# Performance work log

Measured on AMD Instinct MI355X. Metric: run time of the kernel, lower is better.

## Reference

```python
import jax, jax.numpy as jnp
import numpy as np

NEG_INF = -1e9  # fp32-safe mask value for non-edges
ALPHA = 0.2     # LeakyReLU negative slope


def setup_inputs() -> dict:
    key = jax.random.key(0)
    k1, k2, k3, k4, k5 = jax.random.split(key, 5)
    N, F_in, H, F_out = 4096, 512, 8, 64
    features = jax.random.normal(k1, (N, F_in), dtype=jnp.float32)
    adjacency_matrix = jax.random.randint(k2, (N, N), 0, 2, dtype=jnp.int32)
    W = jax.random.normal(k3, (H, F_in, F_out), dtype=jnp.float32) * (F_in ** -0.5)
    a_src = jax.random.normal(k4, (H, F_out), dtype=jnp.float32) * (F_out ** -0.5)
    a_dst = jax.random.normal(k5, (H, F_out), dtype=jnp.float32) * (F_out ** -0.5)
    return {"features": features, "adjacency_matrix": adjacency_matrix,
            "W": W, "a_src": a_src, "a_dst": a_dst}


def reference(features, adjacency_matrix, W, a_src, a_dst):
    # Per-head linear projection: [H, N, F_out]
    Wh = jnp.einsum('nf,hfo->hno', features, W)
    # Attention logits e_ij = LeakyReLU(a_src . Wh_i + a_dst . Wh_j)
    src = jnp.einsum('hno,ho->hn', Wh, a_src)  # [H, N]
    dst = jnp.einsum('hno,ho->hn', Wh, a_dst)  # [H, N]
    e = jax.nn.leaky_relu(src[:, :, None] + dst[:, None, :], ALPHA)  # [H, N, N]
    mask = (adjacency_matrix > 0)[None, :, :]
    e = jnp.where(mask, e, jnp.asarray(NEG_INF, e.dtype))
    attn = jax.nn.softmax(e, axis=-1)  # adjacency-masked row softmax
    h = jnp.einsum('hij,hjo->hio', attn, Wh)  # [H, N, F_out]
    h = jax.nn.elu(h)
    # concat=True: torch.cat over feature dim -> [N, H*F_out]
    return jnp.transpose(h, (1, 0, 2)).reshape(h.shape[1], -1)
```

## Files before the change

kernel.cpp:

```cpp
#include <hip/hip_runtime.h>
#include <hip/hip_bf16.h>

typedef __bf16 bf16x8 __attribute__((ext_vector_type(8)));
typedef float  f32x4  __attribute__((ext_vector_type(4)));
typedef unsigned short u16x8 __attribute__((ext_vector_type(8)));
typedef unsigned short us4   __attribute__((ext_vector_type(4)));

#define HH    8
#define NN    4096
#define FIN   512
#define FOUT  64
#define ALPHA 0.2f

__global__ __launch_bounds__(256) void k_transpose_w(
    const float* __restrict__ Wsrc, __hip_bfloat16* __restrict__ WT) {
    __shared__ __hip_bfloat16 lt[64][65];
    const int h  = blockIdx.x >> 3;
    const int f0 = (blockIdx.x & 7) * 64;
    const int tid = threadIdx.x;
#pragma unroll
    for (int p = 0; p < 16; ++p) {
        int f = p * 4 + (tid >> 6);
        int o = tid & 63;
        lt[f][o] = __float2bfloat16(Wsrc[((size_t)h * FIN + f0 + f) * FOUT + o]);
    }
    __syncthreads();
#pragma unroll
    for (int p = 0; p < 16; ++p) {
        int o = p * 4 + (tid >> 6);
        int f = tid & 63;
        WT[((size_t)h * FOUT + o) * FIN + f0 + f] = lt[f][o];
    }
}

__global__ __launch_bounds__(256) void k_prep(
    int* __restrict__ adj,
    const float* __restrict__ feat,
    const __hip_bfloat16* __restrict__ WT,
    const float* __restrict__ a_src,
    const float* __restrict__ a_dst,
    unsigned short* __restrict__ WhT,
    float* __restrict__ srcv,
    unsigned short* __restrict__ Ebf, unsigned short* __restrict__ Fbf) {
    __shared__ alignas(16) __hip_bfloat16 lfeat[32][520];

    const int tid = threadIdx.x;

    if (blockIdx.x < 2048) {
        const size_t base = (size_t)blockIdx.x * 8192;
        unsigned m = 0;
#pragma unroll
        for (int p = 0; p < 8; ++p) {
            int4 v = *(const int4*)(adj + base + tid * 32 + p * 4);
            m |= (unsigned)(v.x > 0) << (p * 4);
            m |= (unsigned)(v.y > 0) << (p * 4 + 1);
            m |= (unsigned)(v.z > 0) << (p * 4 + 2);
            m |= (unsigned)(v.w > 0) << (p * 4 + 3);
        }
        __syncthreads();
        ((unsigned*)adj)[base + tid] = m;
        return;
    }

    const int pb   = blockIdx.x - 2048;
    const int tile = pb & 127;
    const int hgy  = pb >> 7;

#pragma unroll
    for (int p = 0; p < 16; ++p) {
        int idx  = p * 256 + tid;
        int row  = idx >> 7;
        int col4 = (idx & 127) * 4;
        float4 f = *(const float4*)(feat + (size_t)(tile * 32 + row) * FIN + col4);
        __hip_bfloat16* dst = &lfeat[row][col4];
        dst[0] = __float2bfloat16(f.x); dst[1] = __float2bfloat16(f.y);
        dst[2] = __float2bfloat16(f.z); dst[3] = __float2bfloat16(f.w);
    }
    __syncthreads();

    const int h     = hgy * 4 + (tid >> 6);
    const int lane  = tid & 63;
    const int row16 = lane & 15;
    const int quad  = lane >> 4;

    const unsigned short* WTu = (const unsigned short*)WT + (size_t)h * FOUT * FIN;

    f32x4 acc[2][4] = {};
    for (int k0 = 0; k0 < FIN; k0 += 32) {
        bf16x8 a0 = *(const bf16x8*)&lfeat[row16][k0 + quad * 8];
        bf16x8 a1 = *(const bf16x8*)&lfeat[16 + row16][k0 + quad * 8];
#pragma unroll
        for (int ot = 0; ot < 4; ++ot) {
            bf16x8 b = *(const bf16x8*)(WTu + (size_t)(ot * 16 + row16) * FIN + k0 + quad * 8);
            acc[0][ot] = __builtin_amdgcn_mfma_f32_16x16x32_bf16(a0, b, acc[0][ot], 0, 0, 0);
            acc[1][ot] = __builtin_amdgcn_mfma_f32_16x16x32_bf16(a1, b, acc[1][ot], 0, 0, 0);
        }
    }

#pragma unroll
    for (int g = 0; g < 2; ++g)
#pragma unroll
        for (int ot = 0; ot < 4; ++ot) {
            us4 u;
#pragma unroll
            for (int r = 0; r < 4; ++r)
                u[r] = __builtin_bit_cast(unsigned short, (__bf16)acc[g][ot][r]);
            *(us4*)(WhT + (size_t)(h * FOUT + ot * 16 + row16) * NN
                        + tile * 32 + g * 16 + quad * 4) = u;
        }

    float asv[4], adv[4];
#pragma unroll
    for (int ot = 0; ot < 4; ++ot) {
        asv[ot] = a_src[h * FOUT + ot * 16 + row16];
        adv[ot] = a_dst[h * FOUT + ot * 16 + row16];
    }
#pragma unroll
    for (int g = 0; g < 2; ++g)
#pragma unroll
        for (int r = 0; r < 4; ++r) {
            float ss = 0.f, dd = 0.f;
#pragma unroll
            for (int ot = 0; ot < 4; ++ot) {
                ss += acc[g][ot][r] * asv[ot];
                dd += acc[g][ot][r] * adv[ot];
            }
            ss += __shfl_xor(ss, 1); ss += __shfl_xor(ss, 2);
            ss += __shfl_xor(ss, 4); ss += __shfl_xor(ss, 8);
            dd += __shfl_xor(dd, 1); dd += __shfl_xor(dd, 2);
            dd += __shfl_xor(dd, 4); dd += __shfl_xor(dd, 8);
            if (row16 == 0) {
                int n = tile * 32 + g * 16 + quad * 4 + r;
                srcv[h * NN + n] = ss;
                __bf16 e = (__bf16)__expf(dd);
                __bf16 f = (__bf16)__expf(ALPHA * dd);
                Ebf[h * NN + n] = __builtin_bit_cast(unsigned short, e);
                Fbf[h * NN + n] = __builtin_bit_cast(unsigned short, f);
            }
        }
}

__global__ __launch_bounds__(512, 2) void k_flash(
    const unsigned* __restrict__ maskp,
    const float* __restrict__ srcv,
    const unsigned short* __restrict__ Ebf,
    const unsigned short* __restrict__ Fbf,
    const unsigned short* __restrict__ WhT,
    float* __restrict__ out) {
    __shared__ float st[2][128 * 68];
    __shared__ float lds_l[2][128];

    unsigned* lmask = (unsigned*)&st[0][0];

    const int tid   = threadIdx.x;
    const int seg   = tid >> 6;
    const int lane  = tid & 63;
    const int row16 = lane & 15;
    const int quad  = lane >> 4;
    const int shl   = quad * 8;
    const int tile  = blockIdx.x;
    const int h     = blockIdx.y;

#pragma unroll
    for (int p = 0; p < 8; ++p) {
        int tt = tid + p * 512;
        int c  = tt >> 6;
        int o  = (tt & 63) * 16;
        int4 v = *(const int4*)((const char*)maskp
                                + (size_t)(tile * 64 + c) * 32768 + o);
        int row = c * 2 + (o >> 9);
        int dw  = (o & 511) >> 2;
        *(int4*)&lmask[row * 132 + dw] = v;
    }
    __syncthreads();

    float Es[8], Fs[8];
#pragma unroll
    for (int g = 0; g < 8; ++g) {
        float si = srcv[h * NN + tile * 128 + g * 16 + row16];
        Es[g] = __expf(si);
        Fs[g] = __expf(ALPHA * si);
    }
    const int mbase = row16 * 132 + seg * 16;

    const unsigned short* Eb = Ebf + h * NN + seg * 512;
    const unsigned short* Fb = Fbf + h * NN + seg * 512;
    const unsigned short* wh = WhT + (size_t)h * FOUT * NN + seg * 512;

    f32x4 acc[8][4] = {};
    float lsum[8]   = {};

#pragma unroll 1
    for (int t = 0; t < 16; ++t) {
        int jj = t * 32 + shl;
        u16x8 ev = *(const u16x8*)(Eb + jj);
        u16x8 fv = *(const u16x8*)(Fb + jj);
        bf16x8 b[4];
#pragma unroll
        for (int ot = 0; ot < 4; ++ot)
            b[ot] = *(const bf16x8*)(wh + (size_t)(ot * 16 + row16) * NN + jj);

        float ef[8], ff[8];
#pragma unroll
        for (int k = 0; k < 8; ++k) {
            ef[k] = __uint_as_float((unsigned)ev[k] << 16);
            ff[k] = __uint_as_float((unsigned)fv[k] << 16);
        }

#pragma unroll
        for (int gp = 0; gp < 4; ++gp) {
            const int g0 = gp * 2, g1 = g0 + 1;
            unsigned mb0 = (lmask[mbase + g0 * 2112 + t] >> shl) & 0xffu;
            unsigned mb1 = (lmask[mbase + g1 * 2112 + t] >> shl) & 0xffu;
            union { bf16x8 v8; __hip_bfloat162 h2[4]; } a0u, a1u;
#pragma unroll
            for (int kk = 0; kk < 4; ++kk) {
                const int ka = kk * 2, kb = ka + 1;
                float p0a = ((mb0 >> ka) & 1u) ? fmaxf(ef[ka] * Es[g0], ff[ka] * Fs[g0]) : 0.f;
                float p0b = ((mb0 >> kb) & 1u) ? fmaxf(ef[kb] * Es[g0], ff[kb] * Fs[g0]) : 0.f;
                float p1a = ((mb1 >> ka) & 1u) ? fmaxf(ef[ka] * Es[g1], ff[ka] * Fs[g1]) : 0.f;
                float p1b = ((mb1 >> kb) & 1u) ? fmaxf(ef[kb] * Es[g1], ff[kb] * Fs[g1]) : 0.f;
                lsum[g0] += p0a + p0b;
                lsum[g1] += p1a + p1b;
                a0u.h2[kk] = __float22bfloat162_rn(make_float2(p0a, p0b));
                a1u.h2[kk] = __float22bfloat162_rn(make_float2(p1a, p1b));
            }
#pragma unroll
            for (int ot = 0; ot < 4; ++ot) {
                acc[g0][ot] = __builtin_amdgcn_mfma_f32_16x16x32_bf16(a0u.v8, b[ot], acc[g0][ot], 0, 0, 0);
                acc[g1][ot] = __builtin_amdgcn_mfma_f32_16x16x32_bf16(a1u.v8, b[ot], acc[g1][ot], 0, 0, 0);
            }
        }
    }

#pragma unroll
    for (int g = 0; g < 8; ++g) {
        lsum[g] += __shfl_xor(lsum[g], 16);
        lsum[g] += __shfl_xor(lsum[g], 32);
    }

    __syncthreads();

    auto stash = [&](int buf) {
#pragma unroll
        for (int g = 0; g < 8; ++g)
#pragma unroll
            for (int ot = 0; ot < 4; ++ot)
#pragma unroll
                for (int r = 0; r < 4; ++r)
                    st[buf][(g * 16 + quad * 4 + r) * 68 + ot * 16 + row16] = acc[g][ot][r];
        if (quad == 0)
#pragma unroll
            for (int g = 0; g < 8; ++g)
                lds_l[buf][g * 16 + row16] = lsum[g];
    };
    auto addin = [&](int buf) {
#pragma unroll
        for (int g = 0; g < 8; ++g) {
#pragma unroll
            for (int ot = 0; ot < 4; ++ot)
#pragma unroll
                for (int r = 0; r < 4; ++r)
                    acc[g][ot][r] += st[buf][(g * 16 + quad * 4 + r) * 68 + ot * 16 + row16];
            lsum[g] += lds_l[buf][g * 16 + row16];
        }
    };

    if (seg == 1) stash(0);
    if (seg == 3) stash(1);
    __syncthreads();
    if (seg == 0) addin(0);
    if (seg == 2) addin(1);
    __syncthreads();
    if (seg == 5) stash(0);
    if (seg == 7) stash(1);
    __syncthreads();
    if (seg == 4) addin(0);
    if (seg == 6) addin(1);
    __syncthreads();
    if (seg == 2) stash(0);
    if (seg == 6) stash(1);
    __syncthreads();
    if (seg == 0) addin(0);
    if (seg == 4) addin(1);
    __syncthreads();
    if (seg == 4) stash(0);
    __syncthreads();
    if (seg == 0) {
        addin(0);
#pragma unroll
        for (int g = 0; g < 8; ++g)
#pragma unroll
            for (int r = 0; r < 4; ++r) {
                int   qr  = quad * 4 + r;
                float l   = __shfl(lsum[g], qr);
                float rl  = 1.0f / l;
#pragma unroll
                for (int ot = 0; ot < 4; ++ot) {
                    float v = acc[g][ot][r] * rl;
                    float y = v > 0.f ? v : __expf(v) - 1.f;
                    st[0][(g * 16 + qr) * 68 + ot * 16 + row16] = y;
                }
            }
    }
    __syncthreads();
#pragma unroll
    for (int p = 0; p < 4; ++p) {
        int f    = tid + p * 512;
        int row  = f >> 4;
        int col4 = (f & 15) * 4;
        float4 v = *(const float4*)&st[0][row * 68 + col4];
        *(float4*)&out[(size_t)(tile * 128 + row) * (HH * FOUT) + h * FOUT + col4] = v;
    }
}

extern "C" void kernel_launch(void* const* d_in, const int* in_sizes, int n_in,
                              void* d_out, int out_size, void* d_ws, size_t ws_size,
                              hipStream_t stream) {
    const float* features = (const float*)d_in[0];
    int*         adj      = (int*)d_in[1];
    const float* W        = (const float*)d_in[2];
    const float* a_src    = (const float*)d_in[3];
    const float* a_dst    = (const float*)d_in[4];
    float*       out      = (float*)d_out;

    char* ws = (char*)d_ws;
    __hip_bfloat16* WT   = (__hip_bfloat16*)(ws);
    unsigned short* WhT  = (unsigned short*)(ws + (512 << 10));
    float*          srcv = (float*)(ws + (512 << 10) + (4 << 20));
    unsigned short* Ebf  = (unsigned short*)(ws + (512 << 10) + (4 << 20) + (128 << 10));
    unsigned short* Fbf  = (unsigned short*)(ws + (512 << 10) + (4 << 20) + (192 << 10));

    k_transpose_w<<<dim3(64), 256, 0, stream>>>(W, WT);
    k_prep<<<dim3(2048 + 256), 256, 0, stream>>>(adj, features, WT, a_src, a_dst,
                                                 WhT, srcv, Ebf, Fbf);
    k_flash<<<dim3(32, 8), 512, 0, stream>>>((const unsigned*)adj, srcv, Ebf, Fbf,
                                             WhT, out);
}
```

Measured before the change: 171.5 us.

## Split flash kernel into 64-row tiles with two row groups per block

The flash kernel now processes 64 query rows per block instead of 128, splitting the 8 waves into 2 row groups of 4 waves, each covering 1024 columns per wave. This doubles the grid to 512 blocks and shrinks each wave's accumulators from 8 to 2 row groups, allowing launch bounds of 4 blocks per SM and a shorter 2-stage LDS reduction. The intent is better CU occupancy and fewer reduction steps. The cost is that each block reloads the E/F/Wh column data for fewer rows, which doubles total reads of those operands.

```diff
diff --git a/kernel.cpp b/kernel.cpp
--- a/kernel.cpp
+++ b/kernel.cpp
@@ -140,20 +140,22 @@
         }
 }
 
-__global__ __launch_bounds__(512, 2) void k_flash(
+__global__ __launch_bounds__(512, 4) void k_flash(
     const unsigned* __restrict__ maskp,
     const float* __restrict__ srcv,
     const unsigned short* __restrict__ Ebf,
     const unsigned short* __restrict__ Fbf,
     const unsigned short* __restrict__ WhT,
     float* __restrict__ out) {
-    __shared__ float st[2][128 * 68];
-    __shared__ float lds_l[2][128];
+    __shared__ float st[4][32 * 68];
+    __shared__ float lds_l[4][32];
 
     unsigned* lmask = (unsigned*)&st[0][0];
 
     const int tid   = threadIdx.x;
-    const int seg   = tid >> 6;
+    const int wav   = tid >> 6;
+    const int rg    = wav >> 2;
+    const int seg   = wav & 3;
     const int lane  = tid & 63;
     const int row16 = lane & 15;
     const int quad  = lane >> 4;
@@ -162,36 +164,36 @@
     const int h     = blockIdx.y;
 
 #pragma unroll
-    for (int p = 0; p < 8; ++p) {
+    for (int p = 0; p < 4; ++p) {
         int tt = tid + p * 512;
         int c  = tt >> 6;
         int o  = (tt & 63) * 16;
         int4 v = *(const int4*)((const char*)maskp
-                                + (size_t)(tile * 64 + c) * 32768 + o);
+                                + (size_t)(tile * 32 + c) * 32768 + o);
         int row = c * 2 + (o >> 9);
         int dw  = (o & 511) >> 2;
         *(int4*)&lmask[row * 132 + dw] = v;
     }
     __syncthreads();
 
-    float Es[8], Fs[8];
-#pragma unroll
-    for (int g = 0; g < 8; ++g) {
-        float si = srcv[h * NN + tile * 128 + g * 16 + row16];
+    float Es[2], Fs[2];
+#pragma unroll
+    for (int g = 0; g < 2; ++g) {
+        float si = srcv[h * NN + tile * 64 + rg * 32 + g * 16 + row16];
         Es[g] = __expf(si);
         Fs[g] = __expf(ALPHA * si);
     }
-    const int mbase = row16 * 132 + seg * 16;
-
-    const unsigned short* Eb = Ebf + h * NN + seg * 512;
-    const unsigned short* Fb = Fbf + h * NN + seg * 512;
-    const unsigned short* wh = WhT + (size_t)h * FOUT * NN + seg * 512;
-
-    f32x4 acc[8][4] = {};
-    float lsum[8]   = {};
+    const int mbase = (rg * 32 + row16) * 132 + seg * 32;
+
+    const unsigned short* Eb = Ebf + h * NN + seg * 1024;
+    const unsigned short* Fb = Fbf + h * NN + seg * 1024;
+    const unsigned short* wh = WhT + (size_t)h * FOUT * NN + seg * 1024;
+
+    f32x4 acc[2][4] = {};
+    float lsum[2]   = {};
 
 #pragma unroll 1
-    for (int t = 0; t < 16; ++t) {
+    for (int t = 0; t < 32; ++t) {
         int jj = t * 32 + shl;
         u16x8 ev = *(const u16x8*)(Eb + jj);
         u16x8 fv = *(const u16x8*)(Fb + jj);
@@ -207,56 +209,52 @@
             ff[k] = __uint_as_float((unsigned)fv[k] << 16);
         }
 
-#pragma unroll
-        for (int gp = 0; gp < 4; ++gp) {
-            const int g0 = gp * 2, g1 = g0 + 1;
-            unsigned mb0 = (lmask[mbase + g0 * 2112 + t] >> shl) & 0xffu;
-            unsigned mb1 = (lmask[mbase + g1 * 2112 + t] >> shl) & 0xffu;
-            union { bf16x8 v8; __hip_bfloat162 h2[4]; } a0u, a1u;
-#pragma unroll
-            for (int kk = 0; kk < 4; ++kk) {
-                const int ka = kk * 2, kb = ka + 1;
-                float p0a = ((mb0 >> ka) & 1u) ? fmaxf(ef[ka] * Es[g0], ff[ka] * Fs[g0]) : 0.f;
-                float p0b = ((mb0 >> kb) & 1u) ? fmaxf(ef[kb] * Es[g0], ff[kb] * Fs[g0]) : 0.f;
-                float p1a = ((mb1 >> ka) & 1u) ? fmaxf(ef[ka] * Es[g1], ff[ka] * Fs[g1]) : 0.f;
-                float p1b = ((mb1 >> kb) & 1u) ? fmaxf(ef[kb] * Es[g1], ff[kb] * Fs[g1]) : 0.f;
-                lsum[g0] += p0a + p0b;
-                lsum[g1] += p1a + p1b;
-                a0u.h2[kk] = __float22bfloat162_rn(make_float2(p0a, p0b));
-                a1u.h2[kk] = __float22bfloat162_rn(make_float2(p1a, p1b));
-            }
-#pragma unroll
-            for (int ot = 0; ot < 4; ++ot) {
-                acc[g0][ot] = __builtin_amdgcn_mfma_f32_16x16x32_bf16(a0u.v8, b[ot], acc[g0][ot], 0, 0, 0);
-                acc[g1][ot] = __builtin_amdgcn_mfma_f32_16x16x32_bf16(a1u.v8, b[ot], acc[g1][ot], 0, 0, 0);
-            }
-        }
-    }
-
-#pragma unroll
-    for (int g = 0; g < 8; ++g) {
+        unsigned mb0 = (lmask[mbase + t] >> shl) & 0xffu;
+        unsigned mb1 = (lmask[mbase + 2112 + t] >> shl) & 0xffu;
+        union { bf16x8 v8; __hip_bfloat162 h2[4]; } a0u, a1u;
+#pragma unroll
+        for (int kk = 0; kk < 4; ++kk) {
+            const int ka = kk * 2, kb = ka + 1;
+            float p0a = ((mb0 >> ka) & 1u) ? fmaxf(ef[ka] * Es[0], ff[ka] * Fs[0]) : 0.f;
+            float p0b = ((mb0 >> kb) & 1u) ? fmaxf(ef[kb] * Es[0], ff[kb] * Fs[0]) : 0.f;
+            float p1a = ((mb1 >> ka) & 1u) ? fmaxf(ef[ka] * Es[1], ff[ka] * Fs[1]) : 0.f;
+            float p1b = ((mb1 >> kb) & 1u) ? fmaxf(ef[kb] * Es[1], ff[kb] * Fs[1]) : 0.f;
+            lsum[0] += p0a + p0b;
+            lsum[1] += p1a + p1b;
+            a0u.h2[kk] = __float22bfloat162_rn(make_float2(p0a, p0b));
+            a1u.h2[kk] = __float22bfloat162_rn(make_float2(p1a, p1b));
+        }
+#pragma unroll
+        for (int ot = 0; ot < 4; ++ot) {
+            acc[0][ot] = __builtin_amdgcn_mfma_f32_16x16x32_bf16(a0u.v8, b[ot], acc[0][ot], 0, 0, 0);
+            acc[1][ot] = __builtin_amdgcn_mfma_f32_16x16x32_bf16(a1u.v8, b[ot], acc[1][ot], 0, 0, 0);
+        }
+    }
+
+#pragma unroll
+    for (int g = 0; g < 2; ++g) {
         lsum[g] += __shfl_xor(lsum[g], 16);
         lsum[g] += __shfl_xor(lsum[g], 32);
     }
 
     __syncthreads();
 
+    const int slot0 = rg * 2;
+
     auto stash = [&](int buf) {
 #pragma unroll
-        for (int g = 0; g < 8; ++g)
+        for (int g = 0; g < 2; ++g) {
 #pragma unroll
             for (int ot = 0; ot < 4; ++ot)
 #pragma unroll
                 for (int r = 0; r < 4; ++r)
                     st[buf][(g * 16 + quad * 4 + r) * 68 + ot * 16 + row16] = acc[g][ot][r];
-        if (quad == 0)
-#pragma unroll
-            for (int g = 0; g < 8; ++g)
-                lds_l[buf][g * 16 + row16] = lsum[g];
+            if (quad == 0) lds_l[buf][g * 16 + row16] = lsum[g];
+        }
     };
     auto addin = [&](int buf) {
 #pragma unroll
-        for (int g = 0; g < 8; ++g) {
+        for (int g = 0; g < 2; ++g) {
 #pragma unroll
             for (int ot = 0; ot < 4; ++ot)
 #pragma unroll
@@ -266,30 +264,19 @@
         }
     };
 
-    if (seg == 1) stash(0);
-    if (seg == 3) stash(1);
-    __syncthreads();
-    if (seg == 0) addin(0);
-    if (seg == 2) addin(1);
-    __syncthreads();
-    if (seg == 5) stash(0);
-    if (seg == 7) stash(1);
-    __syncthreads();
-    if (seg == 4) addin(0);
-    if (seg == 6) addin(1);
-    __syncthreads();
-    if (seg == 2) stash(0);
-    if (seg == 6) stash(1);
-    __syncthreads();
-    if (seg == 0) addin(0);
-    if (seg == 4) addin(1);
-    __syncthreads();
-    if (seg == 4) stash(0);
+    if (seg == 1) stash(slot0);
+    if (seg == 3) stash(slot0 + 1);
+    __syncthreads();
+    if (seg == 0) addin(slot0);
+    if (seg == 2) addin(slot0 + 1);
+    __syncthreads();
+    if (seg == 2) stash(slot0);
     __syncthreads();
     if (seg == 0) {
-        addin(0);
-#pragma unroll
-        for (int g = 0; g < 8; ++g)
+        addin(slot0);
+        float* fin = &st[0][0];
+#pragma unroll
+        for (int g = 0; g < 2; ++g)
 #pragma unroll
             for (int r = 0; r < 4; ++r) {
                 int   qr  = quad * 4 + r;
@@ -299,18 +286,19 @@
                 for (int ot = 0; ot < 4; ++ot) {
                     float v = acc[g][ot][r] * rl;
                     float y = v > 0.f ? v : __expf(v) - 1.f;
-                    st[0][(g * 16 + qr) * 68 + ot * 16 + row16] = y;
+                    fin[(rg * 32 + g * 16 + qr) * 68 + ot * 16 + row16] = y;
                 }
             }
     }
     __syncthreads();
-#pragma unroll
-    for (int p = 0; p < 4; ++p) {
+    const float* fin = &st[0][0];
+#pragma unroll
+    for (int p = 0; p < 2; ++p) {
         int f    = tid + p * 512;
         int row  = f >> 4;
         int col4 = (f & 15) * 4;
-        float4 v = *(const float4*)&st[0][row * 68 + col4];
-        *(float4*)&out[(size_t)(tile * 128 + row) * (HH * FOUT) + h * FOUT + col4] = v;
+        float4 v = *(const float4*)&fin[row * 68 + col4];
+        *(float4*)&out[(size_t)(tile * 64 + row) * (HH * FOUT) + h * FOUT + col4] = v;
     }
 }
 
@@ -334,6 +322,6 @@
     k_transpose_w<<<dim3(64), 256, 0, stream>>>(W, WT);
     k_prep<<<dim3(2048 + 256), 256, 0, stream>>>(adj, features, WT, a_src, a_dst,
                                                  WhT, srcv, Ebf, Fbf);
-    k_flash<<<dim3(32, 8), 512, 0, stream>>>((const unsigned*)adj, srcv, Ebf, Fbf,
+    k_flash<<<dim3(64, 8), 512, 0, stream>>>((const unsigned*)adj, srcv, Ebf, Fbf,
                                              WhT, out);
 }
```

Measured after the change: 194.2 us. +13.2%, slower.

## Switch attention path to packed fp16 math, halve row tile, stagger mask columns

Applied to the files above, without the earlier changes.

Stores Wh and the exp(dst) factors as fp16 instead of bf16. Probabilities are now computed with packed half2 multiplies and max, masked with bitfield-extracted words, summed via fdot2, and fed to fp16 MFMA, which removes the fp32 unpack and convert work. The flash kernel now handles 64 rows per block instead of 128, doubling the grid and raising the occupancy hint to 4, with smaller LDS and register use. Each segment starts at a staggered mask column to spread LDS bank accesses, and s_setprio wraps the MFMAs. The risk is fp16 range and precision limits on the exp products, plus reloading the E/F/Wh tiles once more per block.

```diff
diff --git a/kernel.cpp b/kernel.cpp
--- a/kernel.cpp
+++ b/kernel.cpp
@@ -2,6 +2,8 @@
 #include <hip/hip_bf16.h>
 
 typedef __bf16 bf16x8 __attribute__((ext_vector_type(8)));
+typedef _Float16 f16x8 __attribute__((ext_vector_type(8)));
+typedef _Float16 f16x2 __attribute__((ext_vector_type(2)));
 typedef float  f32x4  __attribute__((ext_vector_type(4)));
 typedef unsigned short u16x8 __attribute__((ext_vector_type(8)));
 typedef unsigned short us4   __attribute__((ext_vector_type(4)));
@@ -104,7 +106,7 @@
             us4 u;
 #pragma unroll
             for (int r = 0; r < 4; ++r)
-                u[r] = __builtin_bit_cast(unsigned short, (__bf16)acc[g][ot][r]);
+                u[r] = __builtin_bit_cast(unsigned short, (_Float16)acc[g][ot][r]);
             *(us4*)(WhT + (size_t)(h * FOUT + ot * 16 + row16) * NN
                         + tile * 32 + g * 16 + quad * 4) = u;
         }
@@ -132,23 +134,23 @@
             if (row16 == 0) {
                 int n = tile * 32 + g * 16 + quad * 4 + r;
                 srcv[h * NN + n] = ss;
-                __bf16 e = (__bf16)__expf(dd);
-                __bf16 f = (__bf16)__expf(ALPHA * dd);
+                _Float16 e = (_Float16)__expf(dd);
+                _Float16 f = (_Float16)__expf(ALPHA * dd);
                 Ebf[h * NN + n] = __builtin_bit_cast(unsigned short, e);
                 Fbf[h * NN + n] = __builtin_bit_cast(unsigned short, f);
             }
         }
 }
 
-__global__ __launch_bounds__(512, 2) void k_flash(
+__global__ __launch_bounds__(512, 4) void k_flash(
     const unsigned* __restrict__ maskp,
     const float* __restrict__ srcv,
     const unsigned short* __restrict__ Ebf,
     const unsigned short* __restrict__ Fbf,
     const unsigned short* __restrict__ WhT,
     float* __restrict__ out) {
-    __shared__ float st[2][128 * 68];
-    __shared__ float lds_l[2][128];
+    __shared__ float st[2][64 * 68];
+    __shared__ float lds_l[2][64];
 
     unsigned* lmask = (unsigned*)&st[0][0];
 
@@ -162,24 +164,26 @@
     const int h     = blockIdx.y;
 
 #pragma unroll
-    for (int p = 0; p < 8; ++p) {
+    for (int p = 0; p < 4; ++p) {
         int tt = tid + p * 512;
         int c  = tt >> 6;
         int o  = (tt & 63) * 16;
         int4 v = *(const int4*)((const char*)maskp
-                                + (size_t)(tile * 64 + c) * 32768 + o);
+                                + (size_t)(tile * 32 + c) * 32768 + o);
         int row = c * 2 + (o >> 9);
         int dw  = (o & 511) >> 2;
         *(int4*)&lmask[row * 132 + dw] = v;
     }
     __syncthreads();
 
-    float Es[8], Fs[8];
-#pragma unroll
-    for (int g = 0; g < 8; ++g) {
-        float si = srcv[h * NN + tile * 128 + g * 16 + row16];
-        Es[g] = __expf(si);
-        Fs[g] = __expf(ALPHA * si);
+    f16x2 Es2[4], Fs2[4];
+#pragma unroll
+    for (int g = 0; g < 4; ++g) {
+        float si = srcv[h * NN + tile * 64 + g * 16 + row16];
+        _Float16 e = (_Float16)__expf(si);
+        _Float16 f = (_Float16)__expf(ALPHA * si);
+        Es2[g][0] = e; Es2[g][1] = e;
+        Fs2[g][0] = f; Fs2[g][1] = f;
     }
     const int mbase = row16 * 132 + seg * 16;
 
@@ -187,54 +191,55 @@
     const unsigned short* Fb = Fbf + h * NN + seg * 512;
     const unsigned short* wh = WhT + (size_t)h * FOUT * NN + seg * 512;
 
-    f32x4 acc[8][4] = {};
-    float lsum[8]   = {};
+    f32x4 acc[4][4] = {};
+    float lsum[4]   = {};
+    const f16x2 ones2 = {(_Float16)1.0f, (_Float16)1.0f};
+
+    int t = (seg * 2) & 15;
 
 #pragma unroll 1
-    for (int t = 0; t < 16; ++t) {
-        int jj = t * 32 + shl;
-        u16x8 ev = *(const u16x8*)(Eb + jj);
-        u16x8 fv = *(const u16x8*)(Fb + jj);
-        bf16x8 b[4];
+    for (int i = 0; i < 16; ++i) {
+        const int jj = t * 32 + shl;
+        union { f16x8 v8; f16x2 h2[4]; } evu, fvu;
+        evu.v8 = *(const f16x8*)(Eb + jj);
+        fvu.v8 = *(const f16x8*)(Fb + jj);
+        f16x8 b[4];
 #pragma unroll
         for (int ot = 0; ot < 4; ++ot)
-            b[ot] = *(const bf16x8*)(wh + (size_t)(ot * 16 + row16) * NN + jj);
-
-        float ef[8], ff[8];
-#pragma unroll
-        for (int k = 0; k < 8; ++k) {
-            ef[k] = __uint_as_float((unsigned)ev[k] << 16);
-            ff[k] = __uint_as_float((unsigned)fv[k] << 16);
-        }
-
-#pragma unroll
-        for (int gp = 0; gp < 4; ++gp) {
-            const int g0 = gp * 2, g1 = g0 + 1;
-            unsigned mb0 = (lmask[mbase + g0 * 2112 + t] >> shl) & 0xffu;
-            unsigned mb1 = (lmask[mbase + g1 * 2112 + t] >> shl) & 0xffu;
-            union { bf16x8 v8; __hip_bfloat162 h2[4]; } a0u, a1u;
+            b[ot] = *(const f16x8*)(wh + (size_t)(ot * 16 + row16) * NN + jj);
+
+#pragma unroll
+        for (int g = 0; g < 4; ++g) {
+            unsigned mb = lmask[mbase + g * 2112 + t] >> shl;
+            union { f16x8 v8; unsigned w[4]; } au;
 #pragma unroll
             for (int kk = 0; kk < 4; ++kk) {
-                const int ka = kk * 2, kb = ka + 1;
-                float p0a = ((mb0 >> ka) & 1u) ? fmaxf(ef[ka] * Es[g0], ff[ka] * Fs[g0]) : 0.f;
-                float p0b = ((mb0 >> kb) & 1u) ? fmaxf(ef[kb] * Es[g0], ff[kb] * Fs[g0]) : 0.f;
-                float p1a = ((mb1 >> ka) & 1u) ? fmaxf(ef[ka] * Es[g1], ff[ka] * Fs[g1]) : 0.f;
-                float p1b = ((mb1 >> kb) & 1u) ? fmaxf(ef[kb] * Es[g1], ff[kb] * Fs[g1]) : 0.f;
-                lsum[g0] += p0a + p0b;
-                lsum[g1] += p1a + p1b;
-                a0u.h2[kk] = __float22bfloat162_rn(make_float2(p0a, p0b));
-                a1u.h2[kk] = __float22bfloat162_rn(make_float2(p1a, p1b));
+                f16x2 t0 = evu.h2[kk] * Es2[g];
+                f16x2 t1 = fvu.h2[kk] * Fs2[g];
+                f16x2 p2 = __builtin_elementwise_max(t0, t1);
+                unsigned lo = (unsigned)__builtin_amdgcn_sbfe((int)mb, 2 * kk, 1);
+                unsigned hi = (unsigned)__builtin_amdgcn_sbfe((int)mb, 2 * kk + 1, 1);
+                unsigned w  = (lo & 0xFFFFu) | (hi & 0xFFFF0000u);
+                unsigned pw = __builtin_bit_cast(unsigned, p2) & w;
+                f16x2 mp2   = __builtin_bit_cast(f16x2, pw);
+                au.w[kk] = pw;
+#if __has_builtin(__builtin_amdgcn_fdot2)
+                lsum[g] = __builtin_amdgcn_fdot2(mp2, ones2, lsum[g], false);
+#else
+                lsum[g] += (float)mp2[0] + (float)mp2[1];
+#endif
             }
-#pragma unroll
-            for (int ot = 0; ot < 4; ++ot) {
-                acc[g0][ot] = __builtin_amdgcn_mfma_f32_16x16x32_bf16(a0u.v8, b[ot], acc[g0][ot], 0, 0, 0);
-                acc[g1][ot] = __builtin_amdgcn_mfma_f32_16x16x32_bf16(a1u.v8, b[ot], acc[g1][ot], 0, 0, 0);
-            }
-        }
-    }
-
-#pragma unroll
-    for (int g = 0; g < 8; ++g) {
+            __builtin_amdgcn_s_setprio(1);
+#pragma unroll
+            for (int ot = 0; ot < 4; ++ot)
+                acc[g][ot] = __builtin_amdgcn_mfma_f32_16x16x32_f16(au.v8, b[ot], acc[g][ot], 0, 0, 0);
+            __builtin_amdgcn_s_setprio(0);
+        }
+        t = (t + 1) & 15;
+    }
+
+#pragma unroll
+    for (int g = 0; g < 4; ++g) {
         lsum[g] += __shfl_xor(lsum[g], 16);
         lsum[g] += __shfl_xor(lsum[g], 32);
     }
@@ -243,7 +248,7 @@
 
     auto stash = [&](int buf) {
 #pragma unroll
-        for (int g = 0; g < 8; ++g)
+        for (int g = 0; g < 4; ++g)
 #pragma unroll
             for (int ot = 0; ot < 4; ++ot)
 #pragma unroll
@@ -251,12 +256,12 @@
                     st[buf][(g * 16 + quad * 4 + r) * 68 + ot * 16 + row16] = acc[g][ot][r];
         if (quad == 0)
 #pragma unroll
-            for (int g = 0; g < 8; ++g)
+            for (int g = 0; g < 4; ++g)
                 lds_l[buf][g * 16 + row16] = lsum[g];
     };
     auto addin = [&](int buf) {
 #pragma unroll
-        for (int g = 0; g < 8; ++g) {
+        for (int g = 0; g < 4; ++g) {
 #pragma unroll
             for (int ot = 0; ot < 4; ++ot)
 #pragma unroll
@@ -289,7 +294,7 @@
     if (seg == 0) {
         addin(0);
 #pragma unroll
-        for (int g = 0; g < 8; ++g)
+        for (int g = 0; g < 4; ++g)
 #pragma unroll
             for (int r = 0; r < 4; ++r) {
                 int   qr  = quad * 4 + r;
@@ -305,12 +310,12 @@
     }
     __syncthreads();
 #pragma unroll
-    for (int p = 0; p < 4; ++p) {
+    for (int p = 0; p < 2; ++p) {
         int f    = tid + p * 512;
         int row  = f >> 4;
         int col4 = (f & 15) * 4;
         float4 v = *(const float4*)&st[0][row * 68 + col4];
-        *(float4*)&out[(size_t)(tile * 128 + row) * (HH * FOUT) + h * FOUT + col4] = v;
+        *(float4*)&out[(size_t)(tile * 64 + row) * (HH * FOUT) + h * FOUT + col4] = v;
     }
 }
 
@@ -334,6 +339,6 @@
     k_transpose_w<<<dim3(64), 256, 0, stream>>>(W, WT);
     k_prep<<<dim3(2048 + 256), 256, 0, stream>>>(adj, features, WT, a_src, a_dst,
                                                  WhT, srcv, Ebf, Fbf);
-    k_flash<<<dim3(32, 8), 512, 0, stream>>>((const unsigned*)adj, srcv, Ebf, Fbf,
+    k_flash<<<dim3(64, 8), 512, 0, stream>>>((const unsigned*)adj, srcv, Ebf, Fbf,
                                              WhT, out);
 }
```

After: 167.5 us. 1.02x faster.
